# Kernel optimization log

Hardware: AMD Instinct MI355X
Metric: run time of the kernel (lower is better)

Reference implementation:

```python
import jax, jax.numpy as jnp
import numpy as np

# dims (match init_kwargs / input_specs)
B, T, IN, H, OUT, BR = 128, 250, 700, 512, 20, 4
VTH, DT, WARMUP = 1.0, 1.0, 10


@jax.custom_vjp
def spike_fn(v):
    # Heaviside spike with surrogate gradient (ActFun_adp style)
    return (v > 0.0).astype(v.dtype)

def _spike_fwd(v):
    return spike_fn(v), v

def _spike_bwd(v, g):
    gamma, lens = 0.5, 0.5  # gaussian surrogate
    return (g * gamma * jnp.exp(-v * v / (2.0 * lens * lens)),)

spike_fn.defvjp(_spike_fwd, _spike_bwd)


def make_mask(rng, out_dim, in_dim, branch):
    # each output neuron's branch j sees a disjoint random slice of inputs
    m = np.zeros((out_dim * branch, in_dim), np.float32)
    seg = in_dim // branch
    for i in range(out_dim):
        perm = rng.permutation(in_dim)
        for j in range(branch):
            m[i * branch + j, perm[j * seg:(j + 1) * seg]] = 1.0
    return jnp.asarray(m)


def setup_inputs() -> dict:
    key = jax.random.key(0)
    ks = jax.random.split(key, 12)
    rng = np.random.default_rng(0)
    lim1 = 1.0 / np.sqrt(IN)
    lim2 = 1.0 / np.sqrt(H)
    return {
        "x": jax.random.uniform(ks[0], (B, T, IN), dtype=jnp.float32),
        "W1": jax.random.uniform(ks[1], (H * BR, IN), minval=-lim1, maxval=lim1),
        "b1": jax.random.uniform(ks[2], (H * BR,), minval=-lim1, maxval=lim1),
        "tau_m1": jax.random.uniform(ks[3], (H,), minval=0.0, maxval=4.0),
        "tau_n1": jax.random.uniform(ks[4], (H, BR), minval=0.0, maxval=4.0),
        "mask1": make_mask(rng, H, IN, BR),
        "W2": jax.random.uniform(ks[5], (H * BR, H), minval=-lim2, maxval=lim2),
        "b2": jax.random.uniform(ks[6], (H * BR,), minval=-lim2, maxval=lim2),
        "tau_m2": jax.random.uniform(ks[7], (H,), minval=0.0, maxval=4.0),
        "tau_n2": jax.random.uniform(ks[8], (H, BR), minval=0.0, maxval=4.0),
        "mask2": make_mask(rng, H, H, BR),
        "Wo": jax.random.uniform(ks[9], (OUT, H), minval=-lim2, maxval=lim2),
        "bo": jax.random.uniform(ks[10], (OUT,), minval=-lim2, maxval=lim2),
        "tau_mo": jax.random.uniform(ks[11], (OUT,), minval=0.0, maxval=4.0),
    }


def reference(x, W1, b1, tau_m1, tau_n1, mask1, W2, b2, tau_m2, tau_n2, mask2, Wo, bo, tau_mo):
    beta1 = jax.nn.sigmoid(tau_n1)   # [H,BR] dendritic decay
    alpha1 = jax.nn.sigmoid(tau_m1)  # [H]   membrane decay
    beta2 = jax.nn.sigmoid(tau_n2)
    alpha2 = jax.nn.sigmoid(tau_m2)
    alpha_o = jax.nn.sigmoid(tau_mo)  # [OUT]
    Wm1 = W1 * mask1  # dendritic branch connectivity mask
    Wm2 = W2 * mask2
    Bsz = x.shape[0]
    Hd, Br = tau_n1.shape
    Od = tau_mo.shape[0]

    init = (jnp.zeros((Bsz, Hd, Br)), jnp.zeros((Bsz, Hd)), jnp.zeros((Bsz, Hd)),
            jnp.zeros((Bsz, Hd, Br)), jnp.zeros((Bsz, Hd)), jnp.zeros((Bsz, Hd)),
            jnp.zeros((Bsz, Od)))

    def step(c, xt):
        d1, m1, s1, d2, m2, s2, mo = c
        # layer 1: dendritic filter then LIF membrane with soft reset
        d1 = beta1 * d1 + (1.0 - beta1) * (xt @ Wm1.T + b1).reshape(Bsz, Hd, Br)
        m1 = m1 * alpha1 + (1.0 - alpha1) * DT * d1.sum(-1) - VTH * s1
        s1 = spike_fn(m1 - VTH)
        # layer 2
        d2 = beta2 * d2 + (1.0 - beta2) * (s1 @ Wm2.T + b2).reshape(Bsz, Hd, Br)
        m2 = m2 * alpha2 + (1.0 - alpha2) * DT * d2.sum(-1) - VTH * s2
        s2 = spike_fn(m2 - VTH)
        # leaky readout integrator (no spiking)
        mo = mo * alpha_o + (1.0 - alpha_o) * DT * (s2 @ Wo.T + bo)
        return (d1, m1, s1, d2, m2, s2, mo), jax.nn.softmax(mo, axis=1)

    _, ys = jax.lax.scan(step, init, jnp.swapaxes(x, 0, 1))  # ys: [T,B,OUT]
    # readout_mode == 'sum_softmax': skip steps i <= warmup_steps, sum the rest
    return ys[WARMUP + 1:].sum(0)
```

## Files before the change

### kernel.cpp

```cpp
#include <hip/hip_runtime.h>
#include <math.h>
#include <stdint.h>

#define B_    128
#define T_    250
#define IN_   700
#define INP_  704
#define H_    512
#define OUT_  20
#define BR_   4
#define HB_   2048
#define WARM_ 10
#define VTH_  1.0f
#define TC_   125
#define TP_   128
#define MP_   16384

typedef __attribute__((ext_vector_type(8)))  _Float16 half8;
typedef __attribute__((ext_vector_type(4)))  float f32x4;
typedef __attribute__((ext_vector_type(16))) float f32x16;
typedef __attribute__((ext_vector_type(4)))  int i32x4;
typedef __attribute__((ext_vector_type(16))) int i32x16;
typedef const __attribute__((address_space(1))) void* gptr_t;
typedef __attribute__((address_space(3))) void* lptr_t;

__global__ __launch_bounds__(256)
void w1prep_kernel(const float* __restrict__ W, const float* __restrict__ M,
                   _Float16* __restrict__ w0, _Float16* __restrict__ w1) {
    int i = blockIdx.x * 256 + threadIdx.x;
    if (i >= HB_ * INP_) return;
    int r = i / INP_, c = i - r * INP_;
    float v = (c < IN_) ? W[(size_t)r * IN_ + c] * M[(size_t)r * IN_ + c] : 0.f;
    _Float16 h0 = (_Float16)v;
    w0[i] = h0;
    w1[i] = (_Float16)(v - (float)h0);
}

__global__ __launch_bounds__(256)
void w2prep_kernel(const float* __restrict__ W, const float* __restrict__ M,
                   int8_t* __restrict__ p2, int8_t* __restrict__ p1,
                   int8_t* __restrict__ p0) {
    int i = blockIdx.x * 256 + threadIdx.x;
    if (i >= HB_ * H_) return;
    float v = W[i] * M[i];
    int q = (int)lrintf(v * 67108864.f);
    int b0 = (int)(int8_t)(q & 0xFF);  q = (q - b0) >> 8;
    int b1 = (int)(int8_t)(q & 0xFF);  int b2 = (q - b1) >> 8;
    p0[i] = (int8_t)b0; p1[i] = (int8_t)b1; p2[i] = (int8_t)b2;
}

__global__ __launch_bounds__(256)
void woprep_kernel(const float* __restrict__ Wo, _Float16* __restrict__ wo0,
                   _Float16* __restrict__ wo1) {
    int i = blockIdx.x * 256 + threadIdx.x;
    if (i >= 32 * H_) return;
    int n = i >> 9;
    float v = (n < OUT_) ? Wo[(size_t)n * H_ + (i & (H_ - 1))] : 0.f;
    _Float16 h0 = (_Float16)v;
    wo0[i] = h0;
    wo1[i] = (_Float16)(v - (float)h0);
}

__global__ __launch_bounds__(256)
void convx_kernel(const float* __restrict__ x, _Float16* __restrict__ x0,
                  _Float16* __restrict__ x1, int t0) {
    int i = blockIdx.x * 256 + threadIdx.x;
    if (i >= MP_ * INP_) return;
    int r = i / INP_, c = i - r * INP_;
    int bb = r >> 7, tl = r & (TP_ - 1);
    float v = (tl < TC_ && c < IN_) ? x[((size_t)bb * T_ + t0 + tl) * IN_ + c] : 0.f;
    _Float16 h0 = (_Float16)v;
    x0[i] = h0;
    x1[i] = (_Float16)(v - (float)h0);
}

__global__ void zero_kernel(float* __restrict__ p, int n4) {
    int i = blockIdx.x * blockDim.x + threadIdx.x;
    if (i < n4) ((float4*)p)[i] = make_float4(0.f, 0.f, 0.f, 0.f);
}

__global__ __launch_bounds__(256)
void l1_fused_kernel(const _Float16* __restrict__ x0, const _Float16* __restrict__ x1,
                     const _Float16* __restrict__ w0, const _Float16* __restrict__ w1,
                     const float* __restrict__ bias,
                     float* __restrict__ dst, float* __restrict__ mst,
                     float* __restrict__ spst, int8_t* __restrict__ sout,
                     const float* __restrict__ tau_m, const float* __restrict__ tau_n) {
    __shared__ alignas(16) char SMEM[69632];
    _Float16* S    = (_Float16*)SMEM;
    float*    curS = (float*)SMEM;
    int8_t*   sbuf = (int8_t*)(SMEM + 65536);

    const int tid  = threadIdx.x;
    const int wave = tid >> 6, lane = tid & 63;
    const int bb = blockIdx.y;
    const int bm = bb * TP_, bn = blockIdx.x * 128;

    const int    srow  = tid >> 2;
    const int    skoff = (((tid & 3) ^ ((srow >> 1) & 3)) * 8);
    const size_t aoff0 = (size_t)(bm + srow) * INP_ + skoff;
    const size_t aoff1 = aoff0 + (size_t)64 * INP_;
    const size_t boff0 = (size_t)(bn + srow) * INP_ + skoff;
    const size_t boff1 = boff0 + (size_t)64 * INP_;
    const int lo = wave * 512;

    const int wm = wave & 1, wn = wave >> 1;
    const int row = lane & 31;
    const int khq = lane >> 5;
    const int key = (lane >> 1) & 3;
    const int cK0 = ((0 + khq) ^ key) * 8;
    const int cK1 = ((2 + khq) ^ key) * 8;

    f32x16 acc[2][2] = {};

    auto stage = [&](int kt, int base) {
        const int k0 = kt * 32;
        _Float16* Sb = S + base;
        __builtin_amdgcn_global_load_lds((gptr_t)(x0 + aoff0 + k0), (lptr_t)(Sb + lo),          16, 0, 0);
        __builtin_amdgcn_global_load_lds((gptr_t)(x0 + aoff1 + k0), (lptr_t)(Sb + 2048  + lo),  16, 0, 0);
        __builtin_amdgcn_global_load_lds((gptr_t)(x1 + aoff0 + k0), (lptr_t)(Sb + 4096  + lo),  16, 0, 0);
        __builtin_amdgcn_global_load_lds((gptr_t)(x1 + aoff1 + k0), (lptr_t)(Sb + 6144  + lo),  16, 0, 0);
        __builtin_amdgcn_global_load_lds((gptr_t)(w0 + boff0 + k0), (lptr_t)(Sb + 8192  + lo),  16, 0, 0);
        __builtin_amdgcn_global_load_lds((gptr_t)(w0 + boff1 + k0), (lptr_t)(Sb + 10240 + lo),  16, 0, 0);
        __builtin_amdgcn_global_load_lds((gptr_t)(w1 + boff0 + k0), (lptr_t)(Sb + 12288 + lo),  16, 0, 0);
        __builtin_amdgcn_global_load_lds((gptr_t)(w1 + boff1 + k0), (lptr_t)(Sb + 14336 + lo),  16, 0, 0);
    };

    auto compute = [&](int base) {
        const _Float16* A0b = S + base;
        const _Float16* A1b = A0b + 4096;
        const _Float16* B0b = A0b + 8192;
        const _Float16* B1b = A0b + 12288;
        half8 a0f[2][2], a1f[2][2], b0f[2][2], b1f[2][2];
#pragma unroll
        for (int mt = 0; mt < 2; mt++) {
            const _Float16* ar = &A0b[(wm * 64 + mt * 32 + row) * 32];
            a0f[mt][0] = *(const half8*)&ar[cK0];
            a0f[mt][1] = *(const half8*)&ar[cK1];
        }
#pragma unroll
        for (int nt = 0; nt < 2; nt++) {
            const _Float16* br = &B0b[(wn * 64 + nt * 32 + row) * 32];
            b0f[nt][0] = *(const half8*)&br[cK0];
            b0f[nt][1] = *(const half8*)&br[cK1];
        }
        __builtin_amdgcn_s_setprio(1);
#pragma unroll
        for (int ks = 0; ks < 2; ks++)
#pragma unroll
            for (int mt = 0; mt < 2; mt++)
#pragma unroll
                for (int nt = 0; nt < 2; nt++)
                    acc[mt][nt] = __builtin_amdgcn_mfma_f32_32x32x16_f16(
                        a0f[mt][ks], b0f[nt][ks], acc[mt][nt], 0, 0, 0);
        __builtin_amdgcn_s_setprio(0);
#pragma unroll
        for (int nt = 0; nt < 2; nt++) {
            const _Float16* br = &B1b[(wn * 64 + nt * 32 + row) * 32];
            b1f[nt][0] = *(const half8*)&br[cK0];
            b1f[nt][1] = *(const half8*)&br[cK1];
        }
        __builtin_amdgcn_s_setprio(1);
#pragma unroll
        for (int ks = 0; ks < 2; ks++)
#pragma unroll
            for (int mt = 0; mt < 2; mt++)
#pragma unroll
                for (int nt = 0; nt < 2; nt++)
                    acc[mt][nt] = __builtin_amdgcn_mfma_f32_32x32x16_f16(
                        a0f[mt][ks], b1f[nt][ks], acc[mt][nt], 0, 0, 0);
        __builtin_amdgcn_s_setprio(0);
#pragma unroll
        for (int mt = 0; mt < 2; mt++) {
            const _Float16* ar = &A1b[(wm * 64 + mt * 32 + row) * 32];
            a1f[mt][0] = *(const half8*)&ar[cK0];
            a1f[mt][1] = *(const half8*)&ar[cK1];
        }
        __builtin_amdgcn_s_setprio(1);
#pragma unroll
        for (int ks = 0; ks < 2; ks++)
#pragma unroll
            for (int mt = 0; mt < 2; mt++)
#pragma unroll
                for (int nt = 0; nt < 2; nt++)
                    acc[mt][nt] = __builtin_amdgcn_mfma_f32_32x32x16_f16(
                        a1f[mt][ks], b0f[nt][ks], acc[mt][nt], 0, 0, 0);
        __builtin_amdgcn_s_setprio(0);
    };

    stage(0, 0);
    asm volatile("s_waitcnt vmcnt(0)" ::: "memory");
    __builtin_amdgcn_s_barrier();

    int cur = 0;
    for (int kt = 0; kt < INP_ / 32 - 1; kt++) {
        const int base = cur * 16384;
        stage(kt + 1, base ^ 16384);
        compute(base);
        asm volatile("s_waitcnt vmcnt(0) lgkmcnt(0)" ::: "memory");
        __builtin_amdgcn_s_barrier();
        cur ^= 1;
    }
    compute(cur * 16384);
    __syncthreads();

    const int col = lane & 31;
    const int rb  = 4 * (lane >> 5);
#pragma unroll
    for (int nt = 0; nt < 2; nt++) {
        const int lcol = wn * 64 + nt * 32 + col;
        const float bv = bias[bn + lcol];
#pragma unroll
        for (int mt = 0; mt < 2; mt++) {
#pragma unroll
            for (int reg = 0; reg < 16; reg++) {
                const int trow = wm * 64 + mt * 32 + (reg & 3) + 8 * (reg >> 2) + rb;
                curS[trow * 128 + lcol] = acc[mt][nt][reg] + bv;
            }
        }
    }
    __syncthreads();

    if (tid < 32) {
        const int hg   = blockIdx.x * 32 + tid;
        const int sidx = bb * H_ + hg;
        float alpha = 1.f / (1.f + expf(-tau_m[hg]));
        float4 tn = ((const float4*)tau_n)[hg];
        float4 beta;
        beta.x = 1.f / (1.f + expf(-tn.x));
        beta.y = 1.f / (1.f + expf(-tn.y));
        beta.z = 1.f / (1.f + expf(-tn.z));
        beta.w = 1.f / (1.f + expf(-tn.w));
        float4 d = ((const float4*)dst)[sidx];
        float m = mst[sidx];
        float sp = spst[sidx];
#pragma unroll 5
        for (int t = 0; t < TC_; t++) {
            float4 c = ((const float4*)(curS + t * 128))[tid];
            d.x = beta.x * d.x + (1.f - beta.x) * c.x;
            d.y = beta.y * d.y + (1.f - beta.y) * c.y;
            d.z = beta.z * d.z + (1.f - beta.z) * c.z;
            d.w = beta.w * d.w + (1.f - beta.w) * c.w;
            float s4 = ((d.x + d.y) + d.z) + d.w;
            m = m * alpha + (1.f - alpha) * s4 - VTH_ * sp;
            sp = (m > VTH_) ? 1.f : 0.f;
            sbuf[t * 32 + tid] = (int8_t)(m > VTH_);
        }
        sbuf[125 * 32 + tid] = 0; sbuf[126 * 32 + tid] = 0; sbuf[127 * 32 + tid] = 0;
        ((float4*)dst)[sidx] = d;
        mst[sidx] = m;
        spst[sidx] = sp;
    }
    __syncthreads();
    if (tid < TP_) {
        int4* dp = (int4*)&sout[((size_t)(bm + tid)) * H_ + blockIdx.x * 32];
        const int4* sp4 = (const int4*)&sbuf[tid * 32];
        dp[0] = sp4[0]; dp[1] = sp4[1];
    }
}

__global__ __launch_bounds__(256)
void l2_fused_kernel(const int8_t* __restrict__ A,
                     const int8_t* __restrict__ p2, const int8_t* __restrict__ p1,
                     const int8_t* __restrict__ p0,
                     const float* __restrict__ bias,
                     float* __restrict__ dst, float* __restrict__ mst,
                     float* __restrict__ spst, _Float16* __restrict__ sout,
                     const float* __restrict__ tau_m, const float* __restrict__ tau_n) {
    __shared__ alignas(16) char SMEM[73728];
    int8_t*   S    = (int8_t*)SMEM;
    float*    curS = (float*)SMEM;
    _Float16* sbuf = (_Float16*)(SMEM + 65536);

    const int tid  = threadIdx.x;
    const int wave = tid >> 6, lane = tid & 63;
    const int bb = blockIdx.y;
    const int bm = bb * TP_, bn = blockIdx.x * 128;

    const int    srow  = tid >> 2;
    const int    skoff = (((tid & 3) ^ ((srow >> 1) & 3)) * 16);
    const size_t aoff0 = (size_t)(bm + srow) * H_ + skoff;
    const size_t aoff1 = aoff0 + (size_t)64 * H_;
    const size_t boff0 = (size_t)(bn + srow) * H_ + skoff;
    const size_t boff1 = boff0 + (size_t)64 * H_;
    const int lo = wave * 1024;

    const int wm = wave & 1, wn = wave >> 1;
    const int row = lane & 31;
    const int khq = lane >> 5;
    const int key = (lane >> 1) & 3;
    const int cK0 = ((0 + khq) ^ key) * 16;
    const int cK1 = ((2 + khq) ^ key) * 16;

    i32x16 acc[2][2] = {};

    auto stage = [&](int i, int base) {
        const int s  = i >> 3;
        const int k0 = (i & 7) * 64;
        const int8_t* pw = (s == 0) ? p2 : (s == 1) ? p1 : p0;
        int8_t* Sb = S + base;
        __builtin_amdgcn_global_load_lds((gptr_t)(A  + aoff0 + k0), (lptr_t)(Sb + lo),          16, 0, 0);
        __builtin_amdgcn_global_load_lds((gptr_t)(A  + aoff1 + k0), (lptr_t)(Sb + 4096  + lo),  16, 0, 0);
        __builtin_amdgcn_global_load_lds((gptr_t)(pw + boff0 + k0), (lptr_t)(Sb + 8192  + lo),  16, 0, 0);
        __builtin_amdgcn_global_load_lds((gptr_t)(pw + boff1 + k0), (lptr_t)(Sb + 12288 + lo),  16, 0, 0);
    };

    auto compute = [&](int base) {
        const int8_t* Ab = S + base;
        const int8_t* Bb = Ab + 8192;
        i32x4 af[2][2], bf[2][2];
#pragma unroll
        for (int mt = 0; mt < 2; mt++) {
            const int8_t* ar = &Ab[(wm * 64 + mt * 32 + row) * 64];
            af[mt][0] = *(const i32x4*)&ar[cK0];
            af[mt][1] = *(const i32x4*)&ar[cK1];
        }
#pragma unroll
        for (int nt = 0; nt < 2; nt++) {
            const int8_t* br = &Bb[(wn * 64 + nt * 32 + row) * 64];
            bf[nt][0] = *(const i32x4*)&br[cK0];
            bf[nt][1] = *(const i32x4*)&br[cK1];
        }
        __builtin_amdgcn_s_setprio(1);
#pragma unroll
        for (int ks = 0; ks < 2; ks++)
#pragma unroll
            for (int mt = 0; mt < 2; mt++)
#pragma unroll
                for (int nt = 0; nt < 2; nt++)
                    acc[mt][nt] = __builtin_amdgcn_mfma_i32_32x32x32_i8(
                        af[mt][ks], bf[nt][ks], acc[mt][nt], 0, 0, 0);
        __builtin_amdgcn_s_setprio(0);
    };

    stage(0, 0);
    asm volatile("s_waitcnt vmcnt(0)" ::: "memory");
    __builtin_amdgcn_s_barrier();

    int cur = 0;
    for (int i = 0; i < 23; i++) {
        const int base = cur * 16384;
        stage(i + 1, base ^ 16384);
        if (i == 8 || i == 16) {
#pragma unroll
            for (int mt = 0; mt < 2; mt++)
#pragma unroll
                for (int nt = 0; nt < 2; nt++) acc[mt][nt] *= 256;
        }
        compute(base);
        asm volatile("s_waitcnt vmcnt(0) lgkmcnt(0)" ::: "memory");
        __builtin_amdgcn_s_barrier();
        cur ^= 1;
    }
    compute(cur * 16384);
    __syncthreads();

    const float scale = 1.f / 67108864.f;
    const int col = lane & 31;
    const int rb  = 4 * (lane >> 5);
#pragma unroll
    for (int nt = 0; nt < 2; nt++) {
        const int lcol = wn * 64 + nt * 32 + col;
        const float bv = bias[bn + lcol];
#pragma unroll
        for (int mt = 0; mt < 2; mt++) {
#pragma unroll
            for (int reg = 0; reg < 16; reg++) {
                const int trow = wm * 64 + mt * 32 + (reg & 3) + 8 * (reg >> 2) + rb;
                curS[trow * 128 + lcol] = (float)acc[mt][nt][reg] * scale + bv;
            }
        }
    }
    __syncthreads();

    if (tid < 32) {
        const int hg   = blockIdx.x * 32 + tid;
        const int sidx = bb * H_ + hg;
        float alpha = 1.f / (1.f + expf(-tau_m[hg]));
        float4 tn = ((const float4*)tau_n)[hg];
        float4 beta;
        beta.x = 1.f / (1.f + expf(-tn.x));
        beta.y = 1.f / (1.f + expf(-tn.y));
        beta.z = 1.f / (1.f + expf(-tn.z));
        beta.w = 1.f / (1.f + expf(-tn.w));
        float4 d = ((const float4*)dst)[sidx];
        float m = mst[sidx];
        float sp = spst[sidx];
#pragma unroll 5
        for (int t = 0; t < TC_; t++) {
            float4 c = ((const float4*)(curS + t * 128))[tid];
            d.x = beta.x * d.x + (1.f - beta.x) * c.x;
            d.y = beta.y * d.y + (1.f - beta.y) * c.y;
            d.z = beta.z * d.z + (1.f - beta.z) * c.z;
            d.w = beta.w * d.w + (1.f - beta.w) * c.w;
            float s4 = ((d.x + d.y) + d.z) + d.w;
            m = m * alpha + (1.f - alpha) * s4 - VTH_ * sp;
            sp = (m > VTH_) ? 1.f : 0.f;
            sbuf[t * 32 + tid] = (_Float16)sp;
        }
        sbuf[125 * 32 + tid] = (_Float16)0.f;
        sbuf[126 * 32 + tid] = (_Float16)0.f;
        sbuf[127 * 32 + tid] = (_Float16)0.f;
        ((float4*)dst)[sidx] = d;
        mst[sidx] = m;
        spst[sidx] = sp;
    }
    __syncthreads();
    if (tid < TP_) {
        int4* dp = (int4*)&sout[((size_t)(bm + tid)) * H_ + blockIdx.x * 32];
        const int4* sp4 = (const int4*)&sbuf[tid * 32];
        dp[0] = sp4[0]; dp[1] = sp4[1]; dp[2] = sp4[2]; dp[3] = sp4[3];
    }
}

__global__ __launch_bounds__(256)
void rdot_mfma_kernel(const _Float16* __restrict__ s2c, const _Float16* __restrict__ wo0,
                      const _Float16* __restrict__ wo1, const float* __restrict__ bo,
                      float* __restrict__ curo, int t0) {
    __shared__ alignas(16) _Float16 S[2 * 6144];
    const int tid  = threadIdx.x;
    const int wave = tid >> 6, lane = tid & 63;
    const int bm = blockIdx.x * 128;

    const int    srow  = tid >> 2;
    const int    skoff = (((tid & 3) ^ ((srow >> 1) & 3)) * 8);
    const size_t aoff0 = (size_t)(bm + srow) * H_ + skoff;
    const size_t aoff1 = aoff0 + (size_t)64 * H_;
    const _Float16* bsrc = (wave < 2) ? wo0 : wo1;
    const int bw = wave & 1;
    const size_t boff = (size_t)(bw * 16 + (lane >> 2)) * H_
                      + ((lane & 3) ^ ((lane >> 3) & 3)) * 8;
    const int loA = wave * 512;
    const int loB = 4096 + (wave >> 1) * 1024 + bw * 512;

    const int fr = lane & 15;
    const int key = (lane >> 1) & 3;
    const int cK  = (((lane >> 4) ^ key) * 8);

    f32x4 acc[2][2] = {};

    auto stage = [&](int kt, int base) {
        const int k0 = kt * 32;
        _Float16* Sb = S + base;
        __builtin_amdgcn_global_load_lds((gptr_t)(s2c + aoff0 + k0),  (lptr_t)(Sb + loA),        16, 0, 0);
        __builtin_amdgcn_global_load_lds((gptr_t)(s2c + aoff1 + k0),  (lptr_t)(Sb + 2048 + loA), 16, 0, 0);
        __builtin_amdgcn_global_load_lds((gptr_t)(bsrc + boff + k0),  (lptr_t)(Sb + loB),        16, 0, 0);
    };

    auto compute = [&](int base) {
        const _Float16* Ab  = S + base;
        const _Float16* B0b = Ab + 4096;
        const _Float16* B1b = Ab + 5120;
        half8 af[2], b0[2], b1[2];
#pragma unroll
        for (int mi = 0; mi < 2; mi++)
            af[mi] = *(const half8*)&Ab[(wave * 32 + mi * 16 + fr) * 32 + cK];
#pragma unroll
        for (int ni = 0; ni < 2; ni++) {
            b0[ni] = *(const half8*)&B0b[(ni * 16 + fr) * 32 + cK];
            b1[ni] = *(const half8*)&B1b[(ni * 16 + fr) * 32 + cK];
        }
        __builtin_amdgcn_s_setprio(1);
#pragma unroll
        for (int mi = 0; mi < 2; mi++)
#pragma unroll
            for (int ni = 0; ni < 2; ni++) {
                acc[mi][ni] = __builtin_amdgcn_mfma_f32_16x16x32_f16(af[mi], b0[ni], acc[mi][ni], 0, 0, 0);
                acc[mi][ni] = __builtin_amdgcn_mfma_f32_16x16x32_f16(af[mi], b1[ni], acc[mi][ni], 0, 0, 0);
            }
        __builtin_amdgcn_s_setprio(0);
    };

    stage(0, 0);
    asm volatile("s_waitcnt vmcnt(0)" ::: "memory");
    __builtin_amdgcn_s_barrier();

    int cur = 0;
    for (int kt = 0; kt < H_ / 32 - 1; kt++) {
        const int base = cur * 6144;
        stage(kt + 1, base ^ 6144);
        compute(base);
        asm volatile("s_waitcnt vmcnt(0) lgkmcnt(0)" ::: "memory");
        __builtin_amdgcn_s_barrier();
        cur ^= 1;
    }
    compute(cur * 6144);

    const int cc = lane & 15;
    const int cr = (lane >> 4) * 4;
#pragma unroll
    for (int ni = 0; ni < 2; ni++) {
        const int gc = ni * 16 + cc;
        if (gc < OUT_) {
            const float bv = bo[gc];
#pragma unroll
            for (int mi = 0; mi < 2; mi++) {
#pragma unroll
                for (int r = 0; r < 4; r++) {
                    const int gr = bm + wave * 32 + mi * 16 + cr + r;
                    const int bb = gr >> 7, tl = gr & (TP_ - 1);
                    if (tl < TC_)
                        curo[((size_t)bb * T_ + t0 + tl) * OUT_ + gc] = acc[mi][ni][r] + bv;
                }
            }
        }
    }
}

#define RT_SEG 12
#define RT_LEN 21

__global__ __launch_bounds__(256)
void readout_kernel(const float* __restrict__ curo, const float* __restrict__ tau_mo,
                    float* __restrict__ out) {
    __shared__ float moS[T_ * OUT_];
    __shared__ float segA[RT_SEG][OUT_];
    __shared__ float segU[RT_SEG][OUT_];
    __shared__ float pre[RT_SEG][OUT_];
    __shared__ float accS[OUT_];
    const int b = blockIdx.x;
    const int tid = threadIdx.x;
    const float* cb = curo + (size_t)b * T_ * OUT_;

    const int o = tid % OUT_;
    const int sg = tid / OUT_;
    const float ao = 1.f / (1.f + expf(-tau_mo[o]));

    if (tid < RT_SEG * OUT_) {
        int t0 = sg * RT_LEN;
        int t1 = min(T_, t0 + RT_LEN);
        float u = 0.f, Ap = 1.f;
        for (int t = t0; t < t1; t++) {
            u = ao * u + (1.f - ao) * cb[t * OUT_ + o];
            Ap *= ao;
        }
        segU[sg][o] = u; segA[sg][o] = Ap;
    }
    if (tid < OUT_) accS[tid] = 0.f;
    __syncthreads();
    if (tid < OUT_) {
        float m = 0.f;
        for (int s = 0; s < RT_SEG; s++) {
            pre[s][tid] = m;
            m = segA[s][tid] * m + segU[s][tid];
        }
    }
    __syncthreads();
    if (tid < RT_SEG * OUT_) {
        int t0 = sg * RT_LEN;
        int t1 = min(T_, t0 + RT_LEN);
        float m = pre[sg][o];
        for (int t = t0; t < t1; t++) {
            m = ao * m + (1.f - ao) * cb[t * OUT_ + o];
            moS[t * OUT_ + o] = m;
        }
    }
    __syncthreads();
    if (tid >= WARM_ + 1 && tid < T_) {
        int t = tid;
        float mx = -3.0e38f;
#pragma unroll
        for (int o2 = 0; o2 < OUT_; o2++) mx = fmaxf(mx, moS[t * OUT_ + o2]);
        float es[OUT_]; float se = 0.f;
#pragma unroll
        for (int o2 = 0; o2 < OUT_; o2++) {
            float e = expf(moS[t * OUT_ + o2] - mx);
            es[o2] = e; se += e;
        }
        float inv = 1.f / se;
#pragma unroll
        for (int o2 = 0; o2 < OUT_; o2++) atomicAdd(&accS[o2], es[o2] * inv);
    }
    __syncthreads();
    if (tid < OUT_) out[(size_t)b * OUT_ + tid] = accS[tid];
}

extern "C" void kernel_launch(void* const* d_in, const int* in_sizes, int n_in,
                              void* d_out, int out_size, void* d_ws, size_t ws_size,
                              hipStream_t stream) {
    const float* x      = (const float*)d_in[0];
    const float* W1     = (const float*)d_in[1];
    const float* b1     = (const float*)d_in[2];
    const float* tau_m1 = (const float*)d_in[3];
    const float* tau_n1 = (const float*)d_in[4];
    const float* mask1  = (const float*)d_in[5];
    const float* W2     = (const float*)d_in[6];
    const float* b2     = (const float*)d_in[7];
    const float* tau_m2 = (const float*)d_in[8];
    const float* tau_n2 = (const float*)d_in[9];
    const float* mask2  = (const float*)d_in[10];
    const float* Wo     = (const float*)d_in[11];
    const float* bo     = (const float*)d_in[12];
    const float* tau_mo = (const float*)d_in[13];
    float* out = (float*)d_out;

    char* p = (char*)d_ws;
    auto alloc = [&](size_t bytes) { char* r = p; p += (bytes + 255) & ~(size_t)255; return r; };
    _Float16* w10 = (_Float16*)alloc((size_t)HB_ * INP_ * 2);
    _Float16* w11 = (_Float16*)alloc((size_t)HB_ * INP_ * 2);
    int8_t*   q2  = (int8_t*)alloc((size_t)HB_ * H_);
    int8_t*   q1  = (int8_t*)alloc((size_t)HB_ * H_);
    int8_t*   q0  = (int8_t*)alloc((size_t)HB_ * H_);
    _Float16* wo0 = (_Float16*)alloc((size_t)32 * H_ * 2);
    _Float16* wo1 = (_Float16*)alloc((size_t)32 * H_ * 2);
    _Float16* xc0 = (_Float16*)alloc((size_t)MP_ * INP_ * 2);
    _Float16* xc1 = (_Float16*)alloc((size_t)MP_ * INP_ * 2);
    int8_t*   s1c = (int8_t*)alloc((size_t)MP_ * H_);
    _Float16* s2c = (_Float16*)alloc((size_t)MP_ * H_ * 2);
    float* curo   = (float*)alloc((size_t)B_ * T_ * OUT_ * 4);
    float* st     = (float*)alloc((size_t)786432 * 4);
    float* d1  = st;
    float* m1  = d1 + (size_t)B_ * H_ * BR_;
    float* sp1 = m1 + (size_t)B_ * H_;
    float* d2  = sp1 + (size_t)B_ * H_;
    float* m2  = d2 + (size_t)B_ * H_ * BR_;
    float* sp2 = m2 + (size_t)B_ * H_;

    w1prep_kernel<<<(HB_ * INP_ + 255) / 256, 256, 0, stream>>>(W1, mask1, w10, w11);
    w2prep_kernel<<<(HB_ * H_ + 255) / 256, 256, 0, stream>>>(W2, mask2, q2, q1, q0);
    woprep_kernel<<<(32 * H_ + 255) / 256, 256, 0, stream>>>(Wo, wo0, wo1);
    zero_kernel<<<(786432 / 4 + 255) / 256, 256, 0, stream>>>(st, 786432 / 4);

    dim3 gg(HB_ / 128, B_);
    for (int c = 0; c < 2; c++) {
        const int t0 = c * TC_;
        convx_kernel<<<(MP_ * INP_) / 256, 256, 0, stream>>>(x, xc0, xc1, t0);
        l1_fused_kernel<<<gg, 256, 0, stream>>>(xc0, xc1, w10, w11, b1,
                                                d1, m1, sp1, s1c, tau_m1, tau_n1);
        l2_fused_kernel<<<gg, 256, 0, stream>>>(s1c, q2, q1, q0, b2,
                                                d2, m2, sp2, s2c, tau_m2, tau_n2);
        rdot_mfma_kernel<<<MP_ / 128, 256, 0, stream>>>(s2c, wo0, wo1, bo, curo, t0);
    }
    readout_kernel<<<B_, 256, 0, stream>>>(curo, tau_mo, out);
}
```

Measured before the change: 785.3 us.

## Shrink LDS footprint in layer kernels to raise occupancy

Layer 1 no longer double-buffers the x (A) tiles in LDS. They are loaded into registers and written to a single LDS buffer after a barrier, while W tiles stay double-buffered via direct-to-LDS loads. Both layer kernels now stage the accumulator-to-LDS transfer in four 32-row chunks, so the fp32 current buffer needs 16KB instead of 64KB. Total LDS per block drops, from about 68-72KB to 48KB and 32KB, so more blocks can fit on a CU. The cost is extra barriers per k-step and per chunk, plus more register pressure for the A prefetch.

```diff
diff --git a/kernel.cpp b/kernel.cpp
--- a/kernel.cpp
+++ b/kernel.cpp
@@ -24,6 +24,8 @@
 typedef const __attribute__((address_space(1))) void* gptr_t;
 typedef __attribute__((address_space(3))) void* lptr_t;
 
+#define SB0() __builtin_amdgcn_sched_barrier(0)
+
 __global__ __launch_bounds__(256)
 void w1prep_kernel(const float* __restrict__ W, const float* __restrict__ M,
                    _Float16* __restrict__ w0, _Float16* __restrict__ w1) {
@@ -86,23 +88,22 @@
                      float* __restrict__ dst, float* __restrict__ mst,
                      float* __restrict__ spst, int8_t* __restrict__ sout,
                      const float* __restrict__ tau_m, const float* __restrict__ tau_n) {
-    __shared__ alignas(16) char SMEM[69632];
-    _Float16* S    = (_Float16*)SMEM;
-    float*    curS = (float*)SMEM;
-    int8_t*   sbuf = (int8_t*)(SMEM + 65536);
+    __shared__ alignas(16) char SMEM[49152];
+    float*  curS = (float*)SMEM;
+    int8_t* sbuf = (int8_t*)(SMEM + 16384);
 
     const int tid  = threadIdx.x;
     const int wave = tid >> 6, lane = tid & 63;
     const int bb = blockIdx.y;
     const int bm = bb * TP_, bn = blockIdx.x * 128;
 
-    const int    srow  = tid >> 2;
-    const int    skoff = (((tid & 3) ^ ((srow >> 1) & 3)) * 8);
-    const size_t aoff0 = (size_t)(bm + srow) * INP_ + skoff;
+    const int srow   = tid >> 2;
+    const int chunk  = tid & 3;
+    const int wchunk = chunk ^ ((srow >> 1) & 3);
+    const size_t boff0 = (size_t)(bn + srow) * INP_ + wchunk * 8;
+    const size_t boff1 = boff0 + (size_t)64 * INP_;
+    const size_t aoff0 = (size_t)(bm + srow) * INP_ + chunk * 8;
     const size_t aoff1 = aoff0 + (size_t)64 * INP_;
-    const size_t boff0 = (size_t)(bn + srow) * INP_ + skoff;
-    const size_t boff1 = boff0 + (size_t)64 * INP_;
-    const int lo = wave * 512;
 
     const int wm = wave & 1, wn = wave >> 1;
     const int row = lane & 31;
@@ -112,29 +113,42 @@
     const int cK1 = ((2 + khq) ^ key) * 8;
 
     f32x16 acc[2][2] = {};
-
-    auto stage = [&](int kt, int base) {
+    int4 aR[4];
+
+    auto stageB = [&](int kt, int base) {
         const int k0 = kt * 32;
-        _Float16* Sb = S + base;
-        __builtin_amdgcn_global_load_lds((gptr_t)(x0 + aoff0 + k0), (lptr_t)(Sb + lo),          16, 0, 0);
-        __builtin_amdgcn_global_load_lds((gptr_t)(x0 + aoff1 + k0), (lptr_t)(Sb + 2048  + lo),  16, 0, 0);
-        __builtin_amdgcn_global_load_lds((gptr_t)(x1 + aoff0 + k0), (lptr_t)(Sb + 4096  + lo),  16, 0, 0);
-        __builtin_amdgcn_global_load_lds((gptr_t)(x1 + aoff1 + k0), (lptr_t)(Sb + 6144  + lo),  16, 0, 0);
-        __builtin_amdgcn_global_load_lds((gptr_t)(w0 + boff0 + k0), (lptr_t)(Sb + 8192  + lo),  16, 0, 0);
-        __builtin_amdgcn_global_load_lds((gptr_t)(w0 + boff1 + k0), (lptr_t)(Sb + 10240 + lo),  16, 0, 0);
-        __builtin_amdgcn_global_load_lds((gptr_t)(w1 + boff0 + k0), (lptr_t)(Sb + 12288 + lo),  16, 0, 0);
-        __builtin_amdgcn_global_load_lds((gptr_t)(w1 + boff1 + k0), (lptr_t)(Sb + 14336 + lo),  16, 0, 0);
-    };
-
-    auto compute = [&](int base) {
-        const _Float16* A0b = S + base;
-        const _Float16* A1b = A0b + 4096;
-        const _Float16* B0b = A0b + 8192;
-        const _Float16* B1b = A0b + 12288;
+        char* Sb = SMEM + 16384 + base;
+        __builtin_amdgcn_global_load_lds((gptr_t)(w0 + boff0 + k0), (lptr_t)(Sb + wave * 1024),          16, 0, 0);
+        __builtin_amdgcn_global_load_lds((gptr_t)(w0 + boff1 + k0), (lptr_t)(Sb + 4096  + wave * 1024),  16, 0, 0);
+        __builtin_amdgcn_global_load_lds((gptr_t)(w1 + boff0 + k0), (lptr_t)(Sb + 8192  + wave * 1024),  16, 0, 0);
+        __builtin_amdgcn_global_load_lds((gptr_t)(w1 + boff1 + k0), (lptr_t)(Sb + 12288 + wave * 1024),  16, 0, 0);
+    };
+
+    auto loadA = [&](int kt) {
+        const int k0 = kt * 32;
+        aR[0] = *(const int4*)(x0 + aoff0 + k0);
+        aR[1] = *(const int4*)(x0 + aoff1 + k0);
+        aR[2] = *(const int4*)(x1 + aoff0 + k0);
+        aR[3] = *(const int4*)(x1 + aoff1 + k0);
+    };
+
+    auto writeA = [&]() {
+        char* d = SMEM + srow * 64 + wchunk * 16;
+        *(int4*)(d)         = aR[0];
+        *(int4*)(d + 4096)  = aR[1];
+        *(int4*)(d + 8192)  = aR[2];
+        *(int4*)(d + 12288) = aR[3];
+    };
+
+    auto compute = [&](int bbase) {
+        const _Float16* A0s = (const _Float16*)SMEM;
+        const _Float16* A1s = (const _Float16*)(SMEM + 8192);
+        const _Float16* B0b = (const _Float16*)(SMEM + 16384 + bbase);
+        const _Float16* B1b = (const _Float16*)(SMEM + 16384 + bbase + 8192);
         half8 a0f[2][2], a1f[2][2], b0f[2][2], b1f[2][2];
 #pragma unroll
         for (int mt = 0; mt < 2; mt++) {
-            const _Float16* ar = &A0b[(wm * 64 + mt * 32 + row) * 32];
+            const _Float16* ar = &A0s[(wm * 64 + mt * 32 + row) * 32];
             a0f[mt][0] = *(const half8*)&ar[cK0];
             a0f[mt][1] = *(const half8*)&ar[cK1];
         }
@@ -172,7 +186,7 @@
         __builtin_amdgcn_s_setprio(0);
 #pragma unroll
         for (int mt = 0; mt < 2; mt++) {
-            const _Float16* ar = &A1b[(wm * 64 + mt * 32 + row) * 32];
+            const _Float16* ar = &A1s[(wm * 64 + mt * 32 + row) * 32];
             a1f[mt][0] = *(const half8*)&ar[cK0];
             a1f[mt][1] = *(const half8*)&ar[cK1];
         }
@@ -188,64 +202,80 @@
         __builtin_amdgcn_s_setprio(0);
     };
 
-    stage(0, 0);
+    stageB(0, 0);
+    loadA(0);
+    SB0();
     asm volatile("s_waitcnt vmcnt(0)" ::: "memory");
+    writeA();
+    asm volatile("s_waitcnt lgkmcnt(0)" ::: "memory");
     __builtin_amdgcn_s_barrier();
 
-    int cur = 0;
+#pragma unroll 1
     for (int kt = 0; kt < INP_ / 32 - 1; kt++) {
-        const int base = cur * 16384;
-        stage(kt + 1, base ^ 16384);
-        compute(base);
-        asm volatile("s_waitcnt vmcnt(0) lgkmcnt(0)" ::: "memory");
+        stageB(kt + 1, ((kt + 1) & 1) * 16384);
+        loadA(kt + 1);
+        SB0();
+        compute((kt & 1) * 16384);
         __builtin_amdgcn_s_barrier();
-        cur ^= 1;
-    }
-    compute(cur * 16384);
+        asm volatile("s_waitcnt vmcnt(0)" ::: "memory");
+        writeA();
+        asm volatile("s_waitcnt lgkmcnt(0)" ::: "memory");
+        __builtin_amdgcn_s_barrier();
+    }
+    compute(16384);
     __syncthreads();
 
     const int col = lane & 31;
     const int rb  = 4 * (lane >> 5);
-#pragma unroll
-    for (int nt = 0; nt < 2; nt++) {
-        const int lcol = wn * 64 + nt * 32 + col;
-        const float bv = bias[bn + lcol];
-#pragma unroll
-        for (int mt = 0; mt < 2; mt++) {
-#pragma unroll
-            for (int reg = 0; reg < 16; reg++) {
-                const int trow = wm * 64 + mt * 32 + (reg & 3) + 8 * (reg >> 2) + rb;
-                curS[trow * 128 + lcol] = acc[mt][nt][reg] + bv;
-            }
-        }
-    }
-    __syncthreads();
-
+    const int hg   = blockIdx.x * 32 + (tid & 31);
+    const int sidx = bb * H_ + hg;
+    float alpha = 0.f; float4 beta = {0.f, 0.f, 0.f, 0.f};
+    float4 d = {0.f, 0.f, 0.f, 0.f};
+    float m = 0.f, sp = 0.f;
     if (tid < 32) {
-        const int hg   = blockIdx.x * 32 + tid;
-        const int sidx = bb * H_ + hg;
-        float alpha = 1.f / (1.f + expf(-tau_m[hg]));
+        alpha = 1.f / (1.f + expf(-tau_m[hg]));
         float4 tn = ((const float4*)tau_n)[hg];
-        float4 beta;
         beta.x = 1.f / (1.f + expf(-tn.x));
         beta.y = 1.f / (1.f + expf(-tn.y));
         beta.z = 1.f / (1.f + expf(-tn.z));
         beta.w = 1.f / (1.f + expf(-tn.w));
-        float4 d = ((const float4*)dst)[sidx];
-        float m = mst[sidx];
-        float sp = spst[sidx];
-#pragma unroll 5
-        for (int t = 0; t < TC_; t++) {
-            float4 c = ((const float4*)(curS + t * 128))[tid];
-            d.x = beta.x * d.x + (1.f - beta.x) * c.x;
-            d.y = beta.y * d.y + (1.f - beta.y) * c.y;
-            d.z = beta.z * d.z + (1.f - beta.z) * c.z;
-            d.w = beta.w * d.w + (1.f - beta.w) * c.w;
-            float s4 = ((d.x + d.y) + d.z) + d.w;
-            m = m * alpha + (1.f - alpha) * s4 - VTH_ * sp;
-            sp = (m > VTH_) ? 1.f : 0.f;
-            sbuf[t * 32 + tid] = (int8_t)(m > VTH_);
-        }
+        d  = ((const float4*)dst)[sidx];
+        m  = mst[sidx];
+        sp = spst[sidx];
+    }
+#pragma unroll 1
+    for (int q = 0; q < 4; q++) {
+        if (wm == (q >> 1)) {
+            const int mt = q & 1;
+#pragma unroll
+            for (int nt = 0; nt < 2; nt++) {
+                const int lcol = wn * 64 + nt * 32 + col;
+                const float bv = bias[bn + lcol];
+#pragma unroll
+                for (int reg = 0; reg < 16; reg++) {
+                    const int trow = (reg & 3) + 8 * (reg >> 2) + rb;
+                    curS[trow * 128 + lcol] = acc[mt][nt][reg] + bv;
+                }
+            }
+        }
+        __syncthreads();
+        if (tid < 32) {
+            const int t1 = min(TC_, (q + 1) * 32);
+            for (int t = q * 32; t < t1; t++) {
+                float4 c = ((const float4*)(curS + (t - q * 32) * 128))[tid];
+                d.x = beta.x * d.x + (1.f - beta.x) * c.x;
+                d.y = beta.y * d.y + (1.f - beta.y) * c.y;
+                d.z = beta.z * d.z + (1.f - beta.z) * c.z;
+                d.w = beta.w * d.w + (1.f - beta.w) * c.w;
+                float s4 = ((d.x + d.y) + d.z) + d.w;
+                m = m * alpha + (1.f - alpha) * s4 - VTH_ * sp;
+                sp = (m > VTH_) ? 1.f : 0.f;
+                sbuf[t * 32 + tid] = (int8_t)(m > VTH_);
+            }
+        }
+        __syncthreads();
+    }
+    if (tid < 32) {
         sbuf[125 * 32 + tid] = 0; sbuf[126 * 32 + tid] = 0; sbuf[127 * 32 + tid] = 0;
         ((float4*)dst)[sidx] = d;
         mst[sidx] = m;
@@ -254,8 +284,8 @@
     __syncthreads();
     if (tid < TP_) {
         int4* dp = (int4*)&sout[((size_t)(bm + tid)) * H_ + blockIdx.x * 32];
-        const int4* sp4 = (const int4*)&sbuf[tid * 32];
-        dp[0] = sp4[0]; dp[1] = sp4[1];
+        const int4* s4 = (const int4*)&sbuf[tid * 32];
+        dp[0] = s4[0]; dp[1] = s4[1];
     }
 }
 
@@ -267,10 +297,10 @@
                      float* __restrict__ dst, float* __restrict__ mst,
                      float* __restrict__ spst, _Float16* __restrict__ sout,
                      const float* __restrict__ tau_m, const float* __restrict__ tau_n) {
-    __shared__ alignas(16) char SMEM[73728];
+    __shared__ alignas(16) char SMEM[32768];
     int8_t*   S    = (int8_t*)SMEM;
     float*    curS = (float*)SMEM;
-    _Float16* sbuf = (_Float16*)(SMEM + 65536);
+    _Float16* sbuf = (_Float16*)(SMEM + 16384);
 
     const int tid  = threadIdx.x;
     const int wave = tid >> 6, lane = tid & 63;
@@ -338,6 +368,7 @@
     __builtin_amdgcn_s_barrier();
 
     int cur = 0;
+#pragma unroll 1
     for (int i = 0; i < 23; i++) {
         const int base = cur * 16384;
         stage(i + 1, base ^ 16384);
@@ -358,46 +389,55 @@
     const float scale = 1.f / 67108864.f;
     const int col = lane & 31;
     const int rb  = 4 * (lane >> 5);
-#pragma unroll
-    for (int nt = 0; nt < 2; nt++) {
-        const int lcol = wn * 64 + nt * 32 + col;
-        const float bv = bias[bn + lcol];
-#pragma unroll
-        for (int mt = 0; mt < 2; mt++) {
-#pragma unroll
-            for (int reg = 0; reg < 16; reg++) {
-                const int trow = wm * 64 + mt * 32 + (reg & 3) + 8 * (reg >> 2) + rb;
-                curS[trow * 128 + lcol] = (float)acc[mt][nt][reg] * scale + bv;
-            }
-        }
-    }
-    __syncthreads();
-
+    const int hg   = blockIdx.x * 32 + (tid & 31);
+    const int sidx = bb * H_ + hg;
+    float alpha = 0.f; float4 beta = {0.f, 0.f, 0.f, 0.f};
+    float4 d = {0.f, 0.f, 0.f, 0.f};
+    float m = 0.f, sp = 0.f;
     if (tid < 32) {
-        const int hg   = blockIdx.x * 32 + tid;
-        const int sidx = bb * H_ + hg;
-        float alpha = 1.f / (1.f + expf(-tau_m[hg]));
+        alpha = 1.f / (1.f + expf(-tau_m[hg]));
         float4 tn = ((const float4*)tau_n)[hg];
-        float4 beta;
         beta.x = 1.f / (1.f + expf(-tn.x));
         beta.y = 1.f / (1.f + expf(-tn.y));
         beta.z = 1.f / (1.f + expf(-tn.z));
         beta.w = 1.f / (1.f + expf(-tn.w));
-        float4 d = ((const float4*)dst)[sidx];
-        float m = mst[sidx];
-        float sp = spst[sidx];
-#pragma unroll 5
-        for (int t = 0; t < TC_; t++) {
-            float4 c = ((const float4*)(curS + t * 128))[tid];
-            d.x = beta.x * d.x + (1.f - beta.x) * c.x;
-            d.y = beta.y * d.y + (1.f - beta.y) * c.y;
-            d.z = beta.z * d.z + (1.f - beta.z) * c.z;
-            d.w = beta.w * d.w + (1.f - beta.w) * c.w;
-            float s4 = ((d.x + d.y) + d.z) + d.w;
-            m = m * alpha + (1.f - alpha) * s4 - VTH_ * sp;
-            sp = (m > VTH_) ? 1.f : 0.f;
-            sbuf[t * 32 + tid] = (_Float16)sp;
-        }
+        d  = ((const float4*)dst)[sidx];
+        m  = mst[sidx];
+        sp = spst[sidx];
+    }
+#pragma unroll 1
+    for (int q = 0; q < 4; q++) {
+        if (wm == (q >> 1)) {
+            const int mt = q & 1;
+#pragma unroll
+            for (int nt = 0; nt < 2; nt++) {
+                const int lcol = wn * 64 + nt * 32 + col;
+                const float bv = bias[bn + lcol];
+#pragma unroll
+                for (int reg = 0; reg < 16; reg++) {
+                    const int trow = (reg & 3) + 8 * (reg >> 2) + rb;
+                    curS[trow * 128 + lcol] = (float)acc[mt][nt][reg] * scale + bv;
+                }
+            }
+        }
+        __syncthreads();
+        if (tid < 32) {
+            const int t1 = min(TC_, (q + 1) * 32);
+            for (int t = q * 32; t < t1; t++) {
+                float4 c = ((const float4*)(curS + (t - q * 32) * 128))[tid];
+                d.x = beta.x * d.x + (1.f - beta.x) * c.x;
+                d.y = beta.y * d.y + (1.f - beta.y) * c.y;
+                d.z = beta.z * d.z + (1.f - beta.z) * c.z;
+                d.w = beta.w * d.w + (1.f - beta.w) * c.w;
+                float s4 = ((d.x + d.y) + d.z) + d.w;
+                m = m * alpha + (1.f - alpha) * s4 - VTH_ * sp;
+                sp = (m > VTH_) ? 1.f : 0.f;
+                sbuf[t * 32 + tid] = (_Float16)sp;
+            }
+        }
+        __syncthreads();
+    }
+    if (tid < 32) {
         sbuf[125 * 32 + tid] = (_Float16)0.f;
         sbuf[126 * 32 + tid] = (_Float16)0.f;
         sbuf[127 * 32 + tid] = (_Float16)0.f;
@@ -408,8 +448,8 @@
     __syncthreads();
     if (tid < TP_) {
         int4* dp = (int4*)&sout[((size_t)(bm + tid)) * H_ + blockIdx.x * 32];
-        const int4* sp4 = (const int4*)&sbuf[tid * 32];
-        dp[0] = sp4[0]; dp[1] = sp4[1]; dp[2] = sp4[2]; dp[3] = sp4[3];
+        const int4* s4 = (const int4*)&sbuf[tid * 32];
+        dp[0] = s4[0]; dp[1] = s4[1]; dp[2] = s4[2]; dp[3] = s4[3];
     }
 }
 
```

Result: slower. 1.284 ms (+63.5%).

## Fuse x fp32-to-split-fp16 conversion into layer-1 GEMM operand loading

Applied to the files above, without the earlier changes.

Removes the separate convx kernel that wrote hi/lo fp16 copies of x to a workspace. The layer-1 GEMM now streams raw fp32 x rows straight into LDS with direct global-to-LDS loads, using a swizzled layout, and splits each value into hi/lo fp16 in registers right before the MFMAs. This drops one full write and re-read of the activation workspace per chunk. In exchange it doubles the per-stage LDS footprint and adds conversion ALU work inside the inner loop, which is redone by each of the 16 column blocks that read the same x tile.

```diff
diff --git a/kernel.cpp b/kernel.cpp
--- a/kernel.cpp
+++ b/kernel.cpp
@@ -61,33 +61,19 @@
     wo1[i] = (_Float16)(v - (float)h0);
 }
 
-__global__ __launch_bounds__(256)
-void convx_kernel(const float* __restrict__ x, _Float16* __restrict__ x0,
-                  _Float16* __restrict__ x1, int t0) {
-    int i = blockIdx.x * 256 + threadIdx.x;
-    if (i >= MP_ * INP_) return;
-    int r = i / INP_, c = i - r * INP_;
-    int bb = r >> 7, tl = r & (TP_ - 1);
-    float v = (tl < TC_ && c < IN_) ? x[((size_t)bb * T_ + t0 + tl) * IN_ + c] : 0.f;
-    _Float16 h0 = (_Float16)v;
-    x0[i] = h0;
-    x1[i] = (_Float16)(v - (float)h0);
-}
-
 __global__ void zero_kernel(float* __restrict__ p, int n4) {
     int i = blockIdx.x * blockDim.x + threadIdx.x;
     if (i < n4) ((float4*)p)[i] = make_float4(0.f, 0.f, 0.f, 0.f);
 }
 
 __global__ __launch_bounds__(256)
-void l1_fused_kernel(const _Float16* __restrict__ x0, const _Float16* __restrict__ x1,
+void l1_fused_kernel(const float* __restrict__ x,
                      const _Float16* __restrict__ w0, const _Float16* __restrict__ w1,
-                     const float* __restrict__ bias,
+                     const float* __restrict__ bias, int t0,
                      float* __restrict__ dst, float* __restrict__ mst,
                      float* __restrict__ spst, int8_t* __restrict__ sout,
                      const float* __restrict__ tau_m, const float* __restrict__ tau_n) {
     __shared__ alignas(16) char SMEM[69632];
-    _Float16* S    = (_Float16*)SMEM;
     float*    curS = (float*)SMEM;
     int8_t*   sbuf = (int8_t*)(SMEM + 65536);
 
@@ -98,11 +84,16 @@
 
     const int    srow  = tid >> 2;
     const int    skoff = (((tid & 3) ^ ((srow >> 1) & 3)) * 8);
-    const size_t aoff0 = (size_t)(bm + srow) * INP_ + skoff;
-    const size_t aoff1 = aoff0 + (size_t)64 * INP_;
     const size_t boff0 = (size_t)(bn + srow) * INP_ + skoff;
     const size_t boff1 = boff0 + (size_t)64 * INP_;
-    const int lo = wave * 512;
+
+    const int keyA  = lane >> 3;
+    const int clogA = (lane & 7) ^ keyA;
+    const bool cOOB = (clogA == 7);
+    const float* rowA0 = x + ((size_t)bb * T_ + min(t0 +  0 + wave * 8 + keyA, T_ - 1)) * IN_ + clogA * 4;
+    const float* rowA1 = x + ((size_t)bb * T_ + min(t0 + 32 + wave * 8 + keyA, T_ - 1)) * IN_ + clogA * 4;
+    const float* rowA2 = x + ((size_t)bb * T_ + min(t0 + 64 + wave * 8 + keyA, T_ - 1)) * IN_ + clogA * 4;
+    const float* rowA3 = x + ((size_t)bb * T_ + min(t0 + 96 + wave * 8 + keyA, T_ - 1)) * IN_ + clogA * 4;
 
     const int wm = wave & 1, wn = wave >> 1;
     const int row = lane & 31;
@@ -115,28 +106,50 @@
 
     auto stage = [&](int kt, int base) {
         const int k0 = kt * 32;
-        _Float16* Sb = S + base;
-        __builtin_amdgcn_global_load_lds((gptr_t)(x0 + aoff0 + k0), (lptr_t)(Sb + lo),          16, 0, 0);
-        __builtin_amdgcn_global_load_lds((gptr_t)(x0 + aoff1 + k0), (lptr_t)(Sb + 2048  + lo),  16, 0, 0);
-        __builtin_amdgcn_global_load_lds((gptr_t)(x1 + aoff0 + k0), (lptr_t)(Sb + 4096  + lo),  16, 0, 0);
-        __builtin_amdgcn_global_load_lds((gptr_t)(x1 + aoff1 + k0), (lptr_t)(Sb + 6144  + lo),  16, 0, 0);
-        __builtin_amdgcn_global_load_lds((gptr_t)(w0 + boff0 + k0), (lptr_t)(Sb + 8192  + lo),  16, 0, 0);
-        __builtin_amdgcn_global_load_lds((gptr_t)(w0 + boff1 + k0), (lptr_t)(Sb + 10240 + lo),  16, 0, 0);
-        __builtin_amdgcn_global_load_lds((gptr_t)(w1 + boff0 + k0), (lptr_t)(Sb + 12288 + lo),  16, 0, 0);
-        __builtin_amdgcn_global_load_lds((gptr_t)(w1 + boff1 + k0), (lptr_t)(Sb + 14336 + lo),  16, 0, 0);
+        char* Sb = SMEM + base;
+        const float* a0s = rowA0 + k0;
+        const float* a1s = rowA1 + k0;
+        const float* a2s = rowA2 + k0;
+        const float* a3s = rowA3 + k0;
+        if (kt == INP_ / 32 - 1 && cOOB) { a0s = x; a1s = x; a2s = x; a3s = x; }
+        __builtin_amdgcn_global_load_lds((gptr_t)a0s, (lptr_t)(Sb + 0     + wave * 1024), 16, 0, 0);
+        __builtin_amdgcn_global_load_lds((gptr_t)a1s, (lptr_t)(Sb + 4096  + wave * 1024), 16, 0, 0);
+        __builtin_amdgcn_global_load_lds((gptr_t)a2s, (lptr_t)(Sb + 8192  + wave * 1024), 16, 0, 0);
+        __builtin_amdgcn_global_load_lds((gptr_t)a3s, (lptr_t)(Sb + 12288 + wave * 1024), 16, 0, 0);
+        __builtin_amdgcn_global_load_lds((gptr_t)(w0 + boff0 + k0), (lptr_t)(Sb + 16384 + wave * 1024), 16, 0, 0);
+        __builtin_amdgcn_global_load_lds((gptr_t)(w0 + boff1 + k0), (lptr_t)(Sb + 20480 + wave * 1024), 16, 0, 0);
+        __builtin_amdgcn_global_load_lds((gptr_t)(w1 + boff0 + k0), (lptr_t)(Sb + 24576 + wave * 1024), 16, 0, 0);
+        __builtin_amdgcn_global_load_lds((gptr_t)(w1 + boff1 + k0), (lptr_t)(Sb + 28672 + wave * 1024), 16, 0, 0);
     };
 
     auto compute = [&](int base) {
-        const _Float16* A0b = S + base;
-        const _Float16* A1b = A0b + 4096;
-        const _Float16* B0b = A0b + 8192;
-        const _Float16* B1b = A0b + 12288;
+        const char* Ab = SMEM + base;
+        const _Float16* B0b = (const _Float16*)(SMEM + base + 16384);
+        const _Float16* B1b = (const _Float16*)(SMEM + base + 24576);
         half8 a0f[2][2], a1f[2][2], b0f[2][2], b1f[2][2];
 #pragma unroll
         for (int mt = 0; mt < 2; mt++) {
-            const _Float16* ar = &A0b[(wm * 64 + mt * 32 + row) * 32];
-            a0f[mt][0] = *(const half8*)&ar[cK0];
-            a0f[mt][1] = *(const half8*)&ar[cK1];
+            const int ra = wm * 64 + mt * 32 + row;
+            const char* arow = Ab + ra * 128;
+            const int rk = row & 7;
+#pragma unroll
+            for (int ks = 0; ks < 2; ks++) {
+                const int c0 = ks * 4 + khq * 2;
+                f32x4 lo = *(const f32x4*)(arow + ((c0 ^ rk) << 4));
+                f32x4 hi = *(const f32x4*)(arow + (((c0 + 1) ^ rk) << 4));
+#pragma unroll
+                for (int j = 0; j < 4; j++) {
+                    _Float16 h = (_Float16)lo[j];
+                    a0f[mt][ks][j] = h;
+                    a1f[mt][ks][j] = (_Float16)(lo[j] - (float)h);
+                }
+#pragma unroll
+                for (int j = 0; j < 4; j++) {
+                    _Float16 h = (_Float16)hi[j];
+                    a0f[mt][ks][4 + j] = h;
+                    a1f[mt][ks][4 + j] = (_Float16)(hi[j] - (float)h);
+                }
+            }
         }
 #pragma unroll
         for (int nt = 0; nt < 2; nt++) {
@@ -170,12 +183,6 @@
                     acc[mt][nt] = __builtin_amdgcn_mfma_f32_32x32x16_f16(
                         a0f[mt][ks], b1f[nt][ks], acc[mt][nt], 0, 0, 0);
         __builtin_amdgcn_s_setprio(0);
-#pragma unroll
-        for (int mt = 0; mt < 2; mt++) {
-            const _Float16* ar = &A1b[(wm * 64 + mt * 32 + row) * 32];
-            a1f[mt][0] = *(const half8*)&ar[cK0];
-            a1f[mt][1] = *(const half8*)&ar[cK1];
-        }
         __builtin_amdgcn_s_setprio(1);
 #pragma unroll
         for (int ks = 0; ks < 2; ks++)
@@ -194,14 +201,14 @@
 
     int cur = 0;
     for (int kt = 0; kt < INP_ / 32 - 1; kt++) {
-        const int base = cur * 16384;
-        stage(kt + 1, base ^ 16384);
+        const int base = cur * 32768;
+        stage(kt + 1, base ^ 32768);
         compute(base);
         asm volatile("s_waitcnt vmcnt(0) lgkmcnt(0)" ::: "memory");
         __builtin_amdgcn_s_barrier();
         cur ^= 1;
     }
-    compute(cur * 16384);
+    compute(cur * 32768);
     __syncthreads();
 
     const int col = lane & 31;
@@ -603,8 +610,6 @@
     int8_t*   q0  = (int8_t*)alloc((size_t)HB_ * H_);
     _Float16* wo0 = (_Float16*)alloc((size_t)32 * H_ * 2);
     _Float16* wo1 = (_Float16*)alloc((size_t)32 * H_ * 2);
-    _Float16* xc0 = (_Float16*)alloc((size_t)MP_ * INP_ * 2);
-    _Float16* xc1 = (_Float16*)alloc((size_t)MP_ * INP_ * 2);
     int8_t*   s1c = (int8_t*)alloc((size_t)MP_ * H_);
     _Float16* s2c = (_Float16*)alloc((size_t)MP_ * H_ * 2);
     float* curo   = (float*)alloc((size_t)B_ * T_ * OUT_ * 4);
@@ -624,8 +629,7 @@
     dim3 gg(HB_ / 128, B_);
     for (int c = 0; c < 2; c++) {
         const int t0 = c * TC_;
-        convx_kernel<<<(MP_ * INP_) / 256, 256, 0, stream>>>(x, xc0, xc1, t0);
-        l1_fused_kernel<<<gg, 256, 0, stream>>>(xc0, xc1, w10, w11, b1,
+        l1_fused_kernel<<<gg, 256, 0, stream>>>(x, w10, w11, b1, t0,
                                                 d1, m1, sp1, s1c, tau_m1, tau_n1);
         l2_fused_kernel<<<gg, 256, 0, stream>>>(s1c, q2, q1, q0, b2,
                                                 d2, m2, sp2, s2c, tau_m2, tau_n2);
```

Measured after the change: 799.7 us. About the same (+1.8%).
